# Performance work log

Measured on AMD Instinct MI355X. Metric: run time of the kernel, lower is better.

The kernel has to match this reference:

```python
import jax, jax.numpy as jnp
import numpy as np

RES, RES_, STRIDE = 28, 14, 2
H, KD, AR = 8, 16, 4
SCALE = KD ** -0.5
EPS = 1e-5


def make_bias_idxs(res=RES, res_=RES_, stride=STRIDE):
    pts = [(i, j) for i in range(res) for j in range(res)]
    pts_ = [(i, j) for i in range(res_) for j in range(res_)]
    offs, idxs = {}, []
    for p1 in pts_:
        for p2 in pts:
            off = (abs(p1[0] * stride - p2[0]), abs(p1[1] * stride - p2[1]))
            if off not in offs:
                offs[off] = len(offs)
            idxs.append(offs[off])
    return np.array(idxs, dtype=np.int32).reshape(len(pts_), len(pts)), len(offs)


def setup_inputs() -> dict:
    key = jax.random.key(0)
    ks = jax.random.split(key, 16)
    idxs, n_off = make_bias_idxs()  # n_off == 784
    B, N, C = 128, RES * RES, 256
    d_kv, d_q, d_p, d_pin = 640, 128, 384, 512
    return {
        "hidden_state": jax.random.normal(ks[0], (B, N, C), jnp.float32),
        "w_kv": jax.random.normal(ks[1], (d_kv, C), jnp.float32) * 0.05,
        "kv_gamma": jax.random.uniform(ks[2], (d_kv,), jnp.float32, 0.5, 1.5),
        "kv_beta": jax.random.normal(ks[3], (d_kv,), jnp.float32) * 0.1,
        "kv_mean": jax.random.normal(ks[4], (d_kv,), jnp.float32) * 0.1,
        "kv_var": jax.random.uniform(ks[5], (d_kv,), jnp.float32, 0.5, 1.5),
        "w_q": jax.random.normal(ks[6], (d_q, C), jnp.float32) * 0.05,
        "q_gamma": jax.random.uniform(ks[7], (d_q,), jnp.float32, 0.5, 1.5),
        "q_beta": jax.random.normal(ks[8], (d_q,), jnp.float32) * 0.1,
        "q_mean": jax.random.normal(ks[9], (d_q,), jnp.float32) * 0.1,
        "q_var": jax.random.uniform(ks[10], (d_q,), jnp.float32, 0.5, 1.5),
        "w_proj": jax.random.normal(ks[11], (d_p, d_pin), jnp.float32) * 0.05,
        "p_gamma": jax.random.uniform(ks[12], (d_p,), jnp.float32, 0.5, 1.5),
        "p_beta": jax.random.normal(ks[13], (d_p,), jnp.float32) * 0.1,
        "p_mean": jax.random.normal(ks[14], (d_p,), jnp.float32) * 0.1,
        "p_var": jax.random.uniform(ks[15], (d_p,), jnp.float32, 0.5, 1.5),
        "attention_biases": jax.random.normal(jax.random.fold_in(key, 99), (H, n_off), jnp.float32),
        "attention_bias_idxs": jnp.asarray(idxs),
    }


def _bn(x, gamma, beta, mean, var):
    # eval-mode BatchNorm1d over last dim
    return (x - mean) * (gamma * jax.lax.rsqrt(var + EPS)) + beta


def _hardswish(x):
    return x * jnp.clip(x + 3.0, 0.0, 6.0) * (1.0 / 6.0)


def reference(hidden_state, w_kv, kv_gamma, kv_beta, kv_mean, kv_var,
              w_q, q_gamma, q_beta, q_mean, q_var,
              w_proj, p_gamma, p_beta, p_mean, p_var,
              attention_biases, attention_bias_idxs):
    B, N, C = hidden_state.shape
    N_ = RES_ * RES_
    # kv: [B, N, 640] -> key [B,H,N,KD], value [B,H,N,AR*KD]
    kv = _bn(hidden_state @ w_kv.T, kv_gamma, kv_beta, kv_mean, kv_var)
    kv = kv.reshape(B, N, H, KD + AR * KD)
    k = jnp.transpose(kv[..., :KD], (0, 2, 1, 3))          # [B,H,N,KD]
    v = jnp.transpose(kv[..., KD:], (0, 2, 1, 3))          # [B,H,N,AR*KD]
    # strided query subsample on the spatial grid
    hs = hidden_state.reshape(B, RES, RES, C)[:, ::STRIDE, ::STRIDE].reshape(B, N_, C)
    q = _bn(hs @ w_q.T, q_gamma, q_beta, q_mean, q_var)
    q = jnp.transpose(q.reshape(B, N_, H, KD), (0, 2, 1, 3))  # [B,H,N_,KD]
    bias = attention_biases[:, attention_bias_idxs]           # [H,N_,N] gathered
    attn = jnp.einsum('bhqd,bhkd->bhqk', q, k) * SCALE + bias
    attn = jax.nn.softmax(attn, axis=-1)
    out = jnp.einsum('bhqk,bhkd->bhqd', attn, v)              # [B,H,N_,AR*KD]
    out = jnp.transpose(out, (0, 2, 1, 3)).reshape(B, N_, H * AR * KD)
    out = _bn(_hardswish(out) @ w_proj.T, p_gamma, p_beta, p_mean, p_var)
    return out
```

## Files before the change

### kernel.cpp

```cpp
#include <hip/hip_runtime.h>

typedef _Float16 f16;
typedef __attribute__((ext_vector_type(2))) _Float16 f16x2;
typedef __attribute__((ext_vector_type(4))) _Float16 f16x4;
typedef __attribute__((ext_vector_type(8))) _Float16 f16x8;
typedef __attribute__((ext_vector_type(4))) float fvec4;
typedef __attribute__((ext_vector_type(4))) float f32x4;
typedef __attribute__((ext_vector_type(16))) float f32x16;
typedef __attribute__((ext_vector_type(4))) unsigned int uint4v;

#define NKEY 784
#define NKEYP 800
#define NQ 196
#define NQP 224
#define LOG2E 1.442695041f
#define SC2   0.360673760f
#define THR2  11.5415603f

static __device__ __forceinline__ f32x4 mfma16(f16x8 a, f16x8 b, f32x4 c) {
    return __builtin_amdgcn_mfma_f32_16x16x32_f16(a, b, c, 0, 0, 0);
}
static __device__ __forceinline__ f32x16 mfma32(f16x8 a, f16x8 b, f32x16 c) {
    return __builtin_amdgcn_mfma_f32_32x32x16_f16(a, b, c, 0, 0, 0);
}
static __device__ __forceinline__ unsigned pkrtz(float a, float b) {
    return __builtin_bit_cast(unsigned, __builtin_amdgcn_cvt_pkrtz(a, b));
}
static __device__ __forceinline__ f32x16 z16() {
    f32x16 v;
#pragma unroll
    for (int i = 0; i < 16; ++i) v[i] = 0.f;
    return v;
}

__global__ void prep_scales_all(const float* __restrict__ kg, const float* __restrict__ kb,
                                const float* __restrict__ km, const float* __restrict__ kvv,
                                const float* __restrict__ qg, const float* __restrict__ qb,
                                const float* __restrict__ qm, const float* __restrict__ qv,
                                const float* __restrict__ pg, const float* __restrict__ pb,
                                const float* __restrict__ pm, const float* __restrict__ pv,
                                float* __restrict__ sb) {
    int i = blockIdx.x * 256 + threadIdx.x;
    if (i < 640) {
        float s = kg[i] * rsqrtf(kvv[i] + 1e-5f);
        sb[i] = s; sb[640 + i] = kb[i] - km[i] * s;
    } else if (i < 768) {
        int j = i - 640;
        float s = qg[j] * rsqrtf(qv[j] + 1e-5f);
        sb[1280 + j] = s * SC2;
        sb[1408 + j] = (qb[j] - qm[j] * s) * SC2;
    } else if (i < 1152) {
        int j = i - 768;
        float s = pg[j] * rsqrtf(pv[j] + 1e-5f);
        sb[1536 + j] = s; sb[1920 + j] = pb[j] - pm[j] * s;
    }
}

__global__ void conv_w(const float* __restrict__ wkv, const float* __restrict__ wq,
                       const float* __restrict__ wp, f16* __restrict__ out) {
    int i = blockIdx.x * 256 + threadIdx.x;
    const float* src;
    f16* dst;
    int kc, n, K;
    if (i < 20480)      { int j = i;         kc = j / 640, n = j - kc * 640; src = wkv; dst = out + (size_t)j * 8;            K = 256; }
    else if (i < 24576) { int j = i - 20480; kc = j / 128, n = j - kc * 128; src = wq;  dst = out + 163840 + (size_t)j * 8;   K = 256; }
    else                { int j = i - 24576; kc = j / 384, n = j - kc * 384; src = wp;  dst = out + 196608 + (size_t)j * 8;   K = 512; }
    const float* s = src + (size_t)n * K + kc * 8;
    fvec4 v0 = *(const fvec4*)s;
    fvec4 v1 = *(const fvec4*)(s + 4);
    f16x8 h;
    h[0] = (f16)v0[0]; h[1] = (f16)v0[1]; h[2] = (f16)v0[2]; h[3] = (f16)v0[3];
    h[4] = (f16)v1[0]; h[5] = (f16)v1[1]; h[6] = (f16)v1[2]; h[7] = (f16)v1[3];
    *(f16x8*)dst = h;
}

__global__ void prep_bias(const float* __restrict__ biases, const int* __restrict__ idxs,
                          f16* __restrict__ biasS, int n_off) {
    int tid = blockIdx.x * 256 + threadIdx.x;
    const int r = tid & 15;
    const int lane = (tid >> 4) & 63;
    const int g = tid >> 10;
    const int kbk = g % 25;
    const int tmp = g / 25;
    const int qt = tmp % 7;
    const int h = tmp / 7;
    const int q = qt * 32 + (lane & 31);
    const int key = kbk * 32 + (r & 3) + 8 * (r >> 2) + 4 * (lane >> 5);
    float v;
    if (key >= NKEY)  v = -30000.f;
    else if (q < NQ)  v = biases[h * n_off + idxs[q * NKEY + key]] * LOG2E;
    else              v = 0.f;
    biasS[tid] = (f16)v;
}

template <int MODE>
__global__ __launch_bounds__(256) void gemm_db(
        const void* __restrict__ Ap, const f16x8* __restrict__ Wg,
        const float* __restrict__ sc, const float* __restrict__ sh,
        void* __restrict__ OutA, f16* __restrict__ OutV) {
    constexpr int K     = (MODE == 2) ? 512 : 256;
    constexpr int KS    = K / 32;
    constexpr int CHUNK = (MODE == 2) ? 16 : 32;
    constexpr int NFR   = CHUNK / 16;
    constexpr int NT    = (MODE == 0) ? 640 : (MODE == 1 ? 128 : 384);
    constexpr int NCH   = (MODE == 0) ? 20 : (MODE == 1 ? 4 : 12);
    constexpr int UNITS = (K / 8) * CHUNK;
    constexpr int SR    = UNITS / 256;

    __shared__ f16x8 Wl[2][UNITS];

    const int t = threadIdx.x;
    const int lane = t & 63, wid = t >> 6;
    const int fr = lane & 15, kg = lane >> 4;
    const int m0 = blockIdx.x * 64;
    const int nb0 = blockIdx.y * (NCH * CHUNK);
    const int mrow = m0 + wid * 16 + fr;

    size_t arow;
    if constexpr (MODE == 1) {
        int b = mrow / 196, nn = mrow - b * 196;
        arow = (size_t)b * 784 + (nn / 14) * 56 + (nn % 14) * 2;
    } else {
        arow = (size_t)mrow;
    }
    f16x8 af[KS];
#pragma unroll
    for (int ks = 0; ks < KS; ++ks) {
        if constexpr (MODE == 2) {
            af[ks] = *(const f16x8*)((const f16*)Ap + arow * K + ks * 32 + kg * 8);
        } else {
            const float* a = (const float*)Ap + arow * 256 + ks * 32 + kg * 8;
            fvec4 v0 = *(const fvec4*)a;
            fvec4 v1 = *(const fvec4*)(a + 4);
            f16x8 hv;
            hv[0] = (f16)v0[0]; hv[1] = (f16)v0[1]; hv[2] = (f16)v0[2]; hv[3] = (f16)v0[3];
            hv[4] = (f16)v1[0]; hv[5] = (f16)v1[1]; hv[6] = (f16)v1[2]; hv[7] = (f16)v1[3];
            af[ks] = hv;
        }
    }

#pragma unroll
    for (int rr = 0; rr < SR; ++rr) {
        const int idx = rr * 256 + t;
        Wl[0][idx] = Wg[(size_t)(idx / CHUNK) * NT + nb0 + (idx % CHUNK)];
    }
    __syncthreads();

    const int rg = kg * 4;
    int cur = 0;
    for (int c = 0; c < NCH; ++c) {
        const int n0c = nb0 + c * CHUNK;

        f16x8 nx0, nx1, nx2, nx3;
        if (c + 1 < NCH) {
            const int n0n = n0c + CHUNK;
            nx0 = Wg[(size_t)((0 * 256 + t) / CHUNK) * NT + n0n + ((0 * 256 + t) % CHUNK)];
            if constexpr (SR > 1)
                nx1 = Wg[(size_t)((1 * 256 + t) / CHUNK) * NT + n0n + ((1 * 256 + t) % CHUNK)];
            if constexpr (SR > 2) {
                nx2 = Wg[(size_t)((2 * 256 + t) / CHUNK) * NT + n0n + ((2 * 256 + t) % CHUNK)];
                nx3 = Wg[(size_t)((3 * 256 + t) / CHUNK) * NT + n0n + ((3 * 256 + t) % CHUNK)];
            }
        }

        f32x4 acc[NFR];
#pragma unroll
        for (int j = 0; j < NFR; ++j) acc[j] = (f32x4){0.f, 0.f, 0.f, 0.f};
#pragma unroll
        for (int ks = 0; ks < KS; ++ks) {
            f16x8 bfr[NFR];
#pragma unroll
            for (int nf = 0; nf < NFR; ++nf)
                bfr[nf] = Wl[cur][(ks * 4 + kg) * CHUNK + nf * 16 + fr];
#pragma unroll
            for (int nf = 0; nf < NFR; ++nf)
                acc[nf] = mfma16(af[ks], bfr[nf], acc[nf]);
        }

        const int mbase = m0 + wid * 16 + rg;
#pragma unroll
        for (int nf = 0; nf < NFR; ++nf) {
            const int n = n0c + nf * 16 + fr;
            const float scn = sc[n], shn = sh[n];
            if constexpr (MODE == 0) {
                const int b = mbase / 784;
                const int nn = mbase - b * 784;
                const int hd = n / 80;
                const int cc = n - hd * 80;
                const size_t bh = (size_t)(b * 8 + hd);
                if (cc < 16) {
#pragma unroll
                    for (int r = 0; r < 4; ++r) {
                        float y = acc[nf][r] * scn + shn;
                        ((f16*)OutA)[(bh * NKEYP + nn + r) * 16 + cc] = (f16)y;
                    }
                } else {
                    const int kbk = nn >> 5, sH = (nn >> 4) & 1;
                    const int kq = (nn >> 2) & 3;
                    const int slot = ((((kq & 1) << 1) | (kq >> 1)) << 2) | (nn & 3);
                    f16x4 pv;
#pragma unroll
                    for (int r = 0; r < 4; ++r) pv[r] = (f16)(acc[nf][r] * scn + shn);
                    *(f16x4*)(OutV + ((bh * 25 + kbk) * 2 + sH) * 1024 + (cc - 16) * 16 + slot) = pv;
                }
            } else if constexpr (MODE == 1) {
                const int b = mbase / 196;
                const int nn = mbase - b * 196;
                const int hd = n >> 4, cc = n & 15;
                const size_t bh = (size_t)(b * 8 + hd);
#pragma unroll
                for (int r = 0; r < 4; ++r) {
                    float y = acc[nf][r] * scn + shn;
                    ((f16*)OutA)[(bh * NQP + nn + r) * 16 + cc] = (f16)y;
                }
            } else {
#pragma unroll
                for (int r = 0; r < 4; ++r) {
                    float y = acc[nf][r] * scn + shn;
                    ((float*)OutA)[(size_t)(mbase + r) * 384 + n] = y;
                }
            }
        }

        if (c + 1 < NCH) {
            Wl[cur ^ 1][0 * 256 + t] = nx0;
            if constexpr (SR > 1)
                Wl[cur ^ 1][1 * 256 + t] = nx1;
            if constexpr (SR > 2) {
                Wl[cur ^ 1][2 * 256 + t] = nx2;
                Wl[cur ^ 1][3 * 256 + t] = nx3;
            }
            __syncthreads();
            cur ^= 1;
        }
    }
}

__global__ __launch_bounds__(448) void attn_fused(const f16* __restrict__ kb,
                                                  const f16* __restrict__ vtb,
                                                  const f16* __restrict__ qw,
                                                  const f16* __restrict__ biasS,
                                                  f16* __restrict__ ao) {
    const int bh = blockIdx.x;
    const int b = bh >> 3, h = bh & 7;
    const int wid = threadIdx.x >> 6;
    const int lane = threadIdx.x & 63;
    const int l31 = lane & 31;
    const int hh = lane >> 5;
    const int q0 = wid * 32;

    const f16x8 bq = *(const f16x8*)(qw + ((size_t)bh * NQP + q0 + l31) * 16 + hh * 8);
    const f16* kpp = kb + (size_t)bh * (NKEYP * 16) + (size_t)l31 * 16 + hh * 8;
    const f16* cbp = biasS + ((size_t)(h * 7 + wid) * 25 * 64 + lane) * 16;
    const f16* vkb = vtb + (size_t)bh * 51200 + l31 * 16 + hh * 8;

    float mrun = -1e30f;
    float lsum = 0.f;
    f32x16 o0 = z16(), o1 = z16();

    f32x16 sn;
    {
        const f16x8* bp = (const f16x8*)cbp;
        f16x8 b0 = bp[0], b1 = bp[1];
        f32x16 ci;
#pragma unroll
        for (int r = 0; r < 8; ++r) { ci[r] = (float)b0[r]; ci[8 + r] = (float)b1[r]; }
        sn = mfma32(*(const f16x8*)kpp, bq, ci);
    }

#pragma unroll 1
    for (int kbi = 0; kbi < 25; ++kbi) {
        f32x16 s = sn;
        if (kbi + 1 < 25) {
            kpp += 512; cbp += 1024;
            const f16x8* bp = (const f16x8*)cbp;
            f16x8 b0 = bp[0], b1 = bp[1];
            f32x16 ci;
#pragma unroll
            for (int r = 0; r < 8; ++r) { ci[r] = (float)b0[r]; ci[8 + r] = (float)b1[r]; }
            sn = mfma32(*(const f16x8*)kpp, bq, ci);
        }
        f16x8 bv00 = *(const f16x8*)(vkb);
        f16x8 bv01 = *(const f16x8*)(vkb + 512);
        f16x8 bv10 = *(const f16x8*)(vkb + 1024);
        f16x8 bv11 = *(const f16x8*)(vkb + 1536);
        vkb += 2048;

        float m0v = fmaxf(fmaxf(s[0], s[1]), fmaxf(s[2], s[3]));
        float m1v = fmaxf(fmaxf(s[4], s[5]), fmaxf(s[6], s[7]));
        float m2v = fmaxf(fmaxf(s[8], s[9]), fmaxf(s[10], s[11]));
        float m3v = fmaxf(fmaxf(s[12], s[13]), fmaxf(s[14], s[15]));
        float cmax = fmaxf(fmaxf(m0v, m1v), fmaxf(m2v, m3v));
        cmax = fmaxf(cmax, __shfl_xor(cmax, 32));
        if (__any(cmax > mrun + THR2)) {
            float mnew = fmaxf(mrun, cmax);
            float f = exp2f(mrun - mnew);
            mrun = mnew;
            lsum *= f;
#pragma unroll
            for (int r = 0; r < 16; ++r) {
                const int cr = (r & 3) + ((r >> 2) << 3) + (hh << 2);
                float fr2 = __shfl(f, cr);
                o0[r] *= fr2;
                o1[r] *= fr2;
            }
        }
        float pr[16];
        float psum = 0.f;
#pragma unroll
        for (int r = 0; r < 16; ++r) {
            pr[r] = exp2f(s[r] - mrun);
            psum += pr[r];
        }
        lsum += psum;
        uint4v w0, w1;
        w0[0] = pkrtz(pr[0], pr[1]);   w0[1] = pkrtz(pr[2], pr[3]);
        w0[2] = pkrtz(pr[4], pr[5]);   w0[3] = pkrtz(pr[6], pr[7]);
        w1[0] = pkrtz(pr[8], pr[9]);   w1[1] = pkrtz(pr[10], pr[11]);
        w1[2] = pkrtz(pr[12], pr[13]); w1[3] = pkrtz(pr[14], pr[15]);
        f16x8 pa0 = __builtin_bit_cast(f16x8, w0);
        f16x8 pa1 = __builtin_bit_cast(f16x8, w1);
        o0 = mfma32(pa0, bv00, o0);
        o1 = mfma32(pa0, bv01, o1);
        o0 = mfma32(pa1, bv10, o0);
        o1 = mfma32(pa1, bv11, o1);
    }
    lsum += __shfl_xor(lsum, 32);
    const float inv = 1.0f / lsum;
#pragma unroll
    for (int r = 0; r < 16; ++r) {
        const int cr = (r & 3) + ((r >> 2) << 3) + (hh << 2);
        const float iq = __shfl(inv, cr);
        const int qg = q0 + cr;
        if (qg < NQ) {
            float v0 = o0[r] * iq, v1 = o1[r] * iq;
            float h0 = v0 * fminf(fmaxf(v0 + 3.f, 0.f), 6.f) * (1.f / 6.f);
            float h1 = v1 * fminf(fmaxf(v1 + 3.f, 0.f), 6.f) * (1.f / 6.f);
            f16* dst = ao + ((size_t)b * NQ + qg) * 512 + h * 64 + l31;
            dst[0] = (f16)h0;
            dst[32] = (f16)h1;
        }
    }
}

extern "C" void kernel_launch(void* const* d_in, const int* in_sizes, int n_in,
                              void* d_out, int out_size, void* d_ws, size_t ws_size,
                              hipStream_t stream) {
    (void)n_in; (void)out_size; (void)ws_size;
    const float* hidden = (const float*)d_in[0];
    const float* w_kv   = (const float*)d_in[1];
    const float* w_q    = (const float*)d_in[6];
    const float* w_p    = (const float*)d_in[11];
    const float* biases = (const float*)d_in[16];
    const int*   idxs   = (const int*)d_in[17];
    const int n_off = in_sizes[16] / 8;

    char* ws = (char*)d_ws;
    const size_t OFF_K  = 0;
    const size_t OFF_V  = 26214400;
    const size_t OFF_Q  = 131072000;
    const size_t OFF_AO = 138412032;
    const size_t OFF_W  = 164102144;
    const size_t OFF_SC = 164888576;
    const size_t OFF_BT = 164897792;
    f16*   kbuf  = (f16*)(ws + OFF_K);
    f16*   vbuf  = (f16*)(ws + OFF_V);
    f16*   qbuf  = (f16*)(ws + OFF_Q);
    f16*   aobuf = (f16*)(ws + OFF_AO);
    f16*   wf16  = (f16*)(ws + OFF_W);
    float* scbuf = (float*)(ws + OFF_SC);
    f16*   btbuf = (f16*)(ws + OFF_BT);

    prep_scales_all<<<5, 256, 0, stream>>>(
        (const float*)d_in[2], (const float*)d_in[3], (const float*)d_in[4], (const float*)d_in[5],
        (const float*)d_in[7], (const float*)d_in[8], (const float*)d_in[9], (const float*)d_in[10],
        (const float*)d_in[12], (const float*)d_in[13], (const float*)d_in[14], (const float*)d_in[15],
        scbuf);
    conv_w<<<192, 256, 0, stream>>>(w_kv, w_q, w_p, wf16);
    prep_bias<<<5600, 256, 0, stream>>>(biases, idxs, btbuf, n_off);
    hipMemsetAsync(qbuf, 0, (size_t)1024 * NQP * 16 * 2, stream);
    gemm_db<0><<<dim3(1568, 1), 256, 0, stream>>>(hidden, (const f16x8*)wf16, scbuf, scbuf + 640, kbuf, vbuf);
    gemm_db<1><<<dim3(392, 1), 256, 0, stream>>>(hidden, (const f16x8*)(wf16 + 163840), scbuf + 1280, scbuf + 1408, qbuf, nullptr);
    attn_fused<<<1024, 448, 0, stream>>>(kbuf, vbuf, qbuf, btbuf, aobuf);
    gemm_db<2><<<dim3(392, 2), 256, 0, stream>>>(aobuf, (const f16x8*)(wf16 + 196608), scbuf + 1536, scbuf + 1920, d_out, nullptr);
}
```

Baseline: 210.6 us.

## Merge prep kernels, add 512-thread KV GEMM, tweak attention loop priority

Folds the scale prep, weight conversion, bias gather and the q-buffer memset into one launch to cut launch overhead. Replaces the templated KV projection with a dedicated 512-thread kernel that handles 128 rows per block, so each block shares one weight stream across more rows. In the attention kernel it unrolls the key-block loop by two and raises wave priority around the PV MFMAs. The cost is more register pressure from the unroll, and the merged prep kernel's block count must line up exactly with the q-buffer zero region.

Result: faster. 198.1 us (-6.0%).

```diff
diff --git a/kernel.cpp b/kernel.cpp
--- a/kernel.cpp
+++ b/kernel.cpp
@@ -33,77 +33,172 @@
     return v;
 }
 
-__global__ void prep_scales_all(const float* __restrict__ kg, const float* __restrict__ kb,
-                                const float* __restrict__ km, const float* __restrict__ kvv,
-                                const float* __restrict__ qg, const float* __restrict__ qb,
-                                const float* __restrict__ qm, const float* __restrict__ qv,
-                                const float* __restrict__ pg, const float* __restrict__ pb,
-                                const float* __restrict__ pm, const float* __restrict__ pv,
-                                float* __restrict__ sb) {
-    int i = blockIdx.x * 256 + threadIdx.x;
-    if (i < 640) {
-        float s = kg[i] * rsqrtf(kvv[i] + 1e-5f);
-        sb[i] = s; sb[640 + i] = kb[i] - km[i] * s;
-    } else if (i < 768) {
-        int j = i - 640;
-        float s = qg[j] * rsqrtf(qv[j] + 1e-5f);
-        sb[1280 + j] = s * SC2;
-        sb[1408 + j] = (qb[j] - qm[j] * s) * SC2;
-    } else if (i < 1152) {
-        int j = i - 768;
-        float s = pg[j] * rsqrtf(pv[j] + 1e-5f);
-        sb[1536 + j] = s; sb[1920 + j] = pb[j] - pm[j] * s;
-    }
-}
-
-__global__ void conv_w(const float* __restrict__ wkv, const float* __restrict__ wq,
-                       const float* __restrict__ wp, f16* __restrict__ out) {
-    int i = blockIdx.x * 256 + threadIdx.x;
-    const float* src;
-    f16* dst;
-    int kc, n, K;
-    if (i < 20480)      { int j = i;         kc = j / 640, n = j - kc * 640; src = wkv; dst = out + (size_t)j * 8;            K = 256; }
-    else if (i < 24576) { int j = i - 20480; kc = j / 128, n = j - kc * 128; src = wq;  dst = out + 163840 + (size_t)j * 8;   K = 256; }
-    else                { int j = i - 24576; kc = j / 384, n = j - kc * 384; src = wp;  dst = out + 196608 + (size_t)j * 8;   K = 512; }
-    const float* s = src + (size_t)n * K + kc * 8;
-    fvec4 v0 = *(const fvec4*)s;
-    fvec4 v1 = *(const fvec4*)(s + 4);
-    f16x8 h;
-    h[0] = (f16)v0[0]; h[1] = (f16)v0[1]; h[2] = (f16)v0[2]; h[3] = (f16)v0[3];
-    h[4] = (f16)v1[0]; h[5] = (f16)v1[1]; h[6] = (f16)v1[2]; h[7] = (f16)v1[3];
-    *(f16x8*)dst = h;
-}
-
-__global__ void prep_bias(const float* __restrict__ biases, const int* __restrict__ idxs,
-                          f16* __restrict__ biasS, int n_off) {
-    int tid = blockIdx.x * 256 + threadIdx.x;
-    const int r = tid & 15;
-    const int lane = (tid >> 4) & 63;
-    const int g = tid >> 10;
-    const int kbk = g % 25;
-    const int tmp = g / 25;
-    const int qt = tmp % 7;
-    const int h = tmp / 7;
-    const int q = qt * 32 + (lane & 31);
-    const int key = kbk * 32 + (r & 3) + 8 * (r >> 2) + 4 * (lane >> 5);
-    float v;
-    if (key >= NKEY)  v = -30000.f;
-    else if (q < NQ)  v = biases[h * n_off + idxs[q * NKEY + key]] * LOG2E;
-    else              v = 0.f;
-    biasS[tid] = (f16)v;
+__global__ void prep_all(const float* __restrict__ kg, const float* __restrict__ kbet,
+                         const float* __restrict__ km, const float* __restrict__ kvv,
+                         const float* __restrict__ qg, const float* __restrict__ qbet,
+                         const float* __restrict__ qm, const float* __restrict__ qv,
+                         const float* __restrict__ pg, const float* __restrict__ pbet,
+                         const float* __restrict__ pm, const float* __restrict__ pv,
+                         const float* __restrict__ wkv, const float* __restrict__ wq,
+                         const float* __restrict__ wp, const float* __restrict__ biases,
+                         const int* __restrict__ idxs, int n_off,
+                         float* __restrict__ sb, f16* __restrict__ wf16,
+                         f16* __restrict__ biasS, f16* __restrict__ qbuf) {
+    const int blk = blockIdx.x;
+    const int t = threadIdx.x;
+    if (blk < 5) {
+        int i = blk * 256 + t;
+        if (i < 640) {
+            float s = kg[i] * rsqrtf(kvv[i] + 1e-5f);
+            sb[i] = s; sb[640 + i] = kbet[i] - km[i] * s;
+        } else if (i < 768) {
+            int j = i - 640;
+            float s = qg[j] * rsqrtf(qv[j] + 1e-5f);
+            sb[1280 + j] = s * SC2;
+            sb[1408 + j] = (qbet[j] - qm[j] * s) * SC2;
+        } else if (i < 1152) {
+            int j = i - 768;
+            float s = pg[j] * rsqrtf(pv[j] + 1e-5f);
+            sb[1536 + j] = s; sb[1920 + j] = pbet[j] - pm[j] * s;
+        }
+    } else if (blk < 197) {
+        int i = (blk - 5) * 256 + t;
+        const float* src;
+        f16* dst;
+        int kc, n, K;
+        if (i < 20480)      { int j = i;         kc = j / 640, n = j - kc * 640; src = wkv; dst = wf16 + (size_t)j * 8;          K = 256; }
+        else if (i < 24576) { int j = i - 20480; kc = j / 128, n = j - kc * 128; src = wq;  dst = wf16 + 163840 + (size_t)j * 8; K = 256; }
+        else                { int j = i - 24576; kc = j / 384, n = j - kc * 384; src = wp;  dst = wf16 + 196608 + (size_t)j * 8; K = 512; }
+        const float* s = src + (size_t)n * K + kc * 8;
+        fvec4 v0 = *(const fvec4*)s;
+        fvec4 v1 = *(const fvec4*)(s + 4);
+        f16x8 h;
+        h[0] = (f16)v0[0]; h[1] = (f16)v0[1]; h[2] = (f16)v0[2]; h[3] = (f16)v0[3];
+        h[4] = (f16)v1[0]; h[5] = (f16)v1[1]; h[6] = (f16)v1[2]; h[7] = (f16)v1[3];
+        *(f16x8*)dst = h;
+    } else if (blk < 5797) {
+        int tid = (blk - 197) * 256 + t;
+        const int r = tid & 15;
+        const int lane = (tid >> 4) & 63;
+        const int g = tid >> 10;
+        const int kbk = g % 25;
+        const int tmp = g / 25;
+        const int qt = tmp % 7;
+        const int h = tmp / 7;
+        const int q = qt * 32 + (lane & 31);
+        const int key = kbk * 32 + (r & 3) + 8 * (r >> 2) + 4 * (lane >> 5);
+        float v;
+        if (key >= NKEY)  v = -30000.f;
+        else if (q < NQ)  v = biases[h * n_off + idxs[q * NKEY + key]] * LOG2E;
+        else              v = 0.f;
+        biasS[tid] = (f16)v;
+    } else {
+        int idx = (blk - 5797) * 256 + t;
+        f16x8 zz;
+#pragma unroll
+        for (int j = 0; j < 8; ++j) zz[j] = (f16)0.f;
+        *(f16x8*)(qbuf + (size_t)idx * 8) = zz;
+    }
+}
+
+__global__ __launch_bounds__(512) void gemm_kv(
+        const float* __restrict__ Ap, const f16x8* __restrict__ Wg,
+        const float* __restrict__ sc, const float* __restrict__ sh,
+        f16* __restrict__ OutK, f16* __restrict__ OutV) {
+    __shared__ f16x8 Wl[2][1024];
+
+    const int t = threadIdx.x;
+    const int lane = t & 63, wid = t >> 6;
+    const int fr = lane & 15, kg = lane >> 4;
+    const int m0 = blockIdx.x * 128;
+    const int mrow = m0 + wid * 16 + fr;
+
+    const float* abase = Ap + (size_t)mrow * 256 + kg * 8;
+    f16x8 af[8];
+#pragma unroll
+    for (int ks = 0; ks < 8; ++ks) {
+        fvec4 v0 = *(const fvec4*)(abase + ks * 32);
+        fvec4 v1 = *(const fvec4*)(abase + ks * 32 + 4);
+        f16x8 hv;
+        hv[0] = (f16)v0[0]; hv[1] = (f16)v0[1]; hv[2] = (f16)v0[2]; hv[3] = (f16)v0[3];
+        hv[4] = (f16)v1[0]; hv[5] = (f16)v1[1]; hv[6] = (f16)v1[2]; hv[7] = (f16)v1[3];
+        af[ks] = hv;
+    }
+
+    Wl[0][t]       = Wg[(size_t)(t >> 5) * 640 + (t & 31)];
+    Wl[0][t + 512] = Wg[(size_t)((t + 512) >> 5) * 640 + (t & 31)];
+    __syncthreads();
+
+    const int rg = kg * 4;
+    int cur = 0;
+    for (int c = 0; c < 20; ++c) {
+        const int n0c = c * 32;
+
+        f16x8 nx0, nx1;
+        if (c + 1 < 20) {
+            const int n0n = n0c + 32;
+            nx0 = Wg[(size_t)(t >> 5) * 640 + n0n + (t & 31)];
+            nx1 = Wg[(size_t)((t + 512) >> 5) * 640 + n0n + (t & 31)];
+        }
+
+        f32x4 acc0 = (f32x4){0.f, 0.f, 0.f, 0.f};
+        f32x4 acc1 = (f32x4){0.f, 0.f, 0.f, 0.f};
+#pragma unroll
+        for (int ks = 0; ks < 8; ++ks) {
+            f16x8 b0 = Wl[cur][(ks * 4 + kg) * 32 + fr];
+            f16x8 b1 = Wl[cur][(ks * 4 + kg) * 32 + 16 + fr];
+            acc0 = mfma16(af[ks], b0, acc0);
+            acc1 = mfma16(af[ks], b1, acc1);
+        }
+
+        const int mbase = m0 + wid * 16 + rg;
+#pragma unroll
+        for (int nf = 0; nf < 2; ++nf) {
+            const f32x4 a4 = nf ? acc1 : acc0;
+            const int n = n0c + nf * 16 + fr;
+            const float scn = sc[n], shn = sh[n];
+            const int b = mbase / 784;
+            const int nn = mbase - b * 784;
+            const int hd = n / 80;
+            const int cc = n - hd * 80;
+            const size_t bh = (size_t)(b * 8 + hd);
+            if (cc < 16) {
+#pragma unroll
+                for (int r = 0; r < 4; ++r) {
+                    float y = a4[r] * scn + shn;
+                    OutK[(bh * NKEYP + nn + r) * 16 + cc] = (f16)y;
+                }
+            } else {
+                const int kbk = nn >> 5, sH = (nn >> 4) & 1;
+                const int kq = (nn >> 2) & 3;
+                const int slot = ((((kq & 1) << 1) | (kq >> 1)) << 2) | (nn & 3);
+                f16x4 pv;
+#pragma unroll
+                for (int r = 0; r < 4; ++r) pv[r] = (f16)(a4[r] * scn + shn);
+                *(f16x4*)(OutV + ((bh * 25 + kbk) * 2 + sH) * 1024 + (cc - 16) * 16 + slot) = pv;
+            }
+        }
+
+        if (c + 1 < 20) {
+            Wl[cur ^ 1][t] = nx0;
+            Wl[cur ^ 1][t + 512] = nx1;
+            __syncthreads();
+            cur ^= 1;
+        }
+    }
 }
 
 template <int MODE>
 __global__ __launch_bounds__(256) void gemm_db(
         const void* __restrict__ Ap, const f16x8* __restrict__ Wg,
         const float* __restrict__ sc, const float* __restrict__ sh,
-        void* __restrict__ OutA, f16* __restrict__ OutV) {
+        void* __restrict__ OutA) {
     constexpr int K     = (MODE == 2) ? 512 : 256;
     constexpr int KS    = K / 32;
     constexpr int CHUNK = (MODE == 2) ? 16 : 32;
     constexpr int NFR   = CHUNK / 16;
-    constexpr int NT    = (MODE == 0) ? 640 : (MODE == 1 ? 128 : 384);
-    constexpr int NCH   = (MODE == 0) ? 20 : (MODE == 1 ? 4 : 12);
+    constexpr int NT    = (MODE == 1) ? 128 : 384;
+    constexpr int NCH   = (MODE == 1) ? 4 : 12;
     constexpr int UNITS = (K / 8) * CHUNK;
     constexpr int SR    = UNITS / 256;
 
@@ -182,28 +277,7 @@
         for (int nf = 0; nf < NFR; ++nf) {
             const int n = n0c + nf * 16 + fr;
             const float scn = sc[n], shn = sh[n];
-            if constexpr (MODE == 0) {
-                const int b = mbase / 784;
-                const int nn = mbase - b * 784;
-                const int hd = n / 80;
-                const int cc = n - hd * 80;
-                const size_t bh = (size_t)(b * 8 + hd);
-                if (cc < 16) {
-#pragma unroll
-                    for (int r = 0; r < 4; ++r) {
-                        float y = acc[nf][r] * scn + shn;
-                        ((f16*)OutA)[(bh * NKEYP + nn + r) * 16 + cc] = (f16)y;
-                    }
-                } else {
-                    const int kbk = nn >> 5, sH = (nn >> 4) & 1;
-                    const int kq = (nn >> 2) & 3;
-                    const int slot = ((((kq & 1) << 1) | (kq >> 1)) << 2) | (nn & 3);
-                    f16x4 pv;
-#pragma unroll
-                    for (int r = 0; r < 4; ++r) pv[r] = (f16)(acc[nf][r] * scn + shn);
-                    *(f16x4*)(OutV + ((bh * 25 + kbk) * 2 + sH) * 1024 + (cc - 16) * 16 + slot) = pv;
-                }
-            } else if constexpr (MODE == 1) {
+            if constexpr (MODE == 1) {
                 const int b = mbase / 196;
                 const int nn = mbase - b * 196;
                 const int hd = n >> 4, cc = n & 15;
@@ -268,7 +342,7 @@
         sn = mfma32(*(const f16x8*)kpp, bq, ci);
     }
 
-#pragma unroll 1
+#pragma unroll 2
     for (int kbi = 0; kbi < 25; ++kbi) {
         f32x16 s = sn;
         if (kbi + 1 < 25) {
@@ -320,10 +394,12 @@
         w1[2] = pkrtz(pr[12], pr[13]); w1[3] = pkrtz(pr[14], pr[15]);
         f16x8 pa0 = __builtin_bit_cast(f16x8, w0);
         f16x8 pa1 = __builtin_bit_cast(f16x8, w1);
+        __builtin_amdgcn_s_setprio(1);
         o0 = mfma32(pa0, bv00, o0);
         o1 = mfma32(pa0, bv01, o1);
         o0 = mfma32(pa1, bv10, o0);
         o1 = mfma32(pa1, bv11, o1);
+        __builtin_amdgcn_s_setprio(0);
     }
     lsum += __shfl_xor(lsum, 32);
     const float inv = 1.0f / lsum;
@@ -371,16 +447,13 @@
     float* scbuf = (float*)(ws + OFF_SC);
     f16*   btbuf = (f16*)(ws + OFF_BT);
 
-    prep_scales_all<<<5, 256, 0, stream>>>(
+    prep_all<<<7589, 256, 0, stream>>>(
         (const float*)d_in[2], (const float*)d_in[3], (const float*)d_in[4], (const float*)d_in[5],
         (const float*)d_in[7], (const float*)d_in[8], (const float*)d_in[9], (const float*)d_in[10],
         (const float*)d_in[12], (const float*)d_in[13], (const float*)d_in[14], (const float*)d_in[15],
-        scbuf);
-    conv_w<<<192, 256, 0, stream>>>(w_kv, w_q, w_p, wf16);
-    prep_bias<<<5600, 256, 0, stream>>>(biases, idxs, btbuf, n_off);
-    hipMemsetAsync(qbuf, 0, (size_t)1024 * NQP * 16 * 2, stream);
-    gemm_db<0><<<dim3(1568, 1), 256, 0, stream>>>(hidden, (const f16x8*)wf16, scbuf, scbuf + 640, kbuf, vbuf);
-    gemm_db<1><<<dim3(392, 1), 256, 0, stream>>>(hidden, (const f16x8*)(wf16 + 163840), scbuf + 1280, scbuf + 1408, qbuf, nullptr);
+        w_kv, w_q, w_p, biases, idxs, n_off, scbuf, wf16, btbuf, qbuf);
+    gemm_db<1><<<dim3(392, 1), 256, 0, stream>>>(hidden, (const f16x8*)(wf16 + 163840), scbuf + 1280, scbuf + 1408, qbuf);
+    gemm_kv<<<784, 512, 0, stream>>>(hidden, (const f16x8*)wf16, scbuf, scbuf + 640, kbuf, vbuf);
     attn_fused<<<1024, 448, 0, stream>>>(kbuf, vbuf, qbuf, btbuf, aobuf);
-    gemm_db<2><<<dim3(392, 2), 256, 0, stream>>>(aobuf, (const f16x8*)(wf16 + 196608), scbuf + 1536, scbuf + 1920, d_out, nullptr);
-}
+    gemm_db<2><<<dim3(392, 2), 256, 0, stream>>>(aobuf, (const f16x8*)(wf16 + 196608), scbuf + 1536, scbuf + 1920, d_out);
+}
```
